# Kernel tuning notes

Measured on AMD Instinct MI355X. Metric: run time of the kernel, lower is better.

## Reference

```python
import jax, jax.numpy as jnp
import numpy as np

EPS = float(np.finfo(np.float32).eps)


def setup_inputs() -> dict:
    key = jax.random.key(0)
    k1, k2, k3, k4 = jax.random.split(key, 4)
    B, M, N = 16, 200000, 200000
    xyzs1 = jax.random.normal(k1, (B, M, 3), dtype=jnp.float32)
    xyzs2 = jax.random.normal(k2, (B, M, 3), dtype=jnp.float32)
    pred_pairs = jax.random.randint(k3, (B, N, 2), 0, M)
    weights = jax.random.uniform(k4, (B, 1, N), dtype=jnp.float32)
    return {"xyzs1": xyzs1, "xyzs2": xyzs2, "pred_pairs": pred_pairs, "weights": weights}


def _weighted_procrustes(X, Y, w):
    # X, Y: [B, N, 3]; w: [B, N, 1]. DGR-style weighted Kabsch/Procrustes.
    W1 = jnp.abs(w).sum(axis=1, keepdims=True)            # [B, 1, 1]
    w_norm = w / (W1 + EPS)                               # [B, N, 1]
    mux = (w_norm * X).sum(axis=1, keepdims=True)         # [B, 1, 3]
    muy = (w_norm * Y).sum(axis=1, keepdims=True)         # [B, 1, 3]
    # Sxy = (Y - muy)^T @ (w_norm * (X - mux)) per sample -> [B, 3, 3]
    Sxy = jnp.einsum('bni,bnj->bij', Y - muy, w_norm * (X - mux))
    U, _, Vh = jnp.linalg.svd(Sxy)                        # Sxy = U diag(s) Vh
    # reflection fix: diag(1, 1, sign(det(U) * det(V)))
    d = jnp.where(jnp.linalg.det(U) * jnp.linalg.det(Vh) < 0, -1.0, 1.0)  # [B]
    S = jnp.concatenate([jnp.ones((X.shape[0], 2), dtype=U.dtype), d[:, None]], axis=1)
    R = (U * S[:, None, :]) @ Vh                          # U @ diag(S) @ V^T
    t = muy[:, 0, :] - jnp.einsum('bij,bj->bi', R, mux[:, 0, :])  # [B, 3]
    return R, t


def reference(xyzs1, xyzs2, pred_pairs, weights):
    w = jnp.transpose(weights, (0, 2, 1))                 # [B, N, 1]
    # batched gather of correspondences
    X = jax.vmap(lambda pts, idx: pts[idx])(xyzs1, pred_pairs[:, :, 0])
    Y = jax.vmap(lambda pts, idx: pts[idx])(xyzs2, pred_pairs[:, :, 1])
    Rs, ts = _weighted_procrustes(X, Y, w)
    ws = w.sum(axis=(1, 2))                               # per-sample weight sums
    return Rs, ts, ws
```

## Files before the change

### kernel.cpp

```cpp
#include <hip/hip_runtime.h>
#include <math.h>

#define BPB 128
#define NACC 17

struct __attribute__((packed, aligned(4))) f4 { float x, y, z, w; };

__global__ __launch_bounds__(256) void wp_partials(
    const float* __restrict__ xyzs1,
    const float* __restrict__ xyzs2,
    const int*   __restrict__ pairs,
    const float* __restrict__ weights,
    float* __restrict__ partials,
    int B, int M, int N)
{
    int b, ib;
    if ((B & 7) == 0) {
        const int grp = blockIdx.x / (8 * BPB);
        const int r   = blockIdx.x % (8 * BPB);
        b  = grp * 8 + (r & 7);
        ib = r >> 3;
    } else {
        b  = blockIdx.x % B;
        ib = blockIdx.x / B;
    }
    const int tid = threadIdx.x;

    const float* __restrict__ x1b = xyzs1 + (size_t)b * M * 3;
    const float* __restrict__ x2b = xyzs2 + (size_t)b * M * 3;
    const unsigned long long* __restrict__ pb =
        (const unsigned long long*)(pairs + (size_t)b * N * 2);
    const float* __restrict__ wb  = weights + (size_t)b * N;

    const bool lastBatch = (b == B - 1);
    const int  M1 = M - 1;

    float acc[NACC];
#pragma unroll
    for (int k = 0; k < NACC; ++k) acc[k] = 0.f;

    for (int n = ib * 256 + tid; n < N; n += BPB * 256) {
        const unsigned long long pw = __builtin_nontemporal_load(pb + n);
        const int ix = (int)(unsigned)(pw & 0xffffffffu);
        const int iy = (int)(unsigned)(pw >> 32);
        const float w = __builtin_nontemporal_load(wb + n);

        float X0, X1, X2, Y0, Y1, Y2;
        {
            const size_t o = 3 * (size_t)ix;
            if (__builtin_expect(lastBatch && ix == M1, 0)) {
                X0 = x1b[o]; X1 = x1b[o + 1]; X2 = x1b[o + 2];
            } else {
                const f4 v = *(const f4*)(x1b + o);
                X0 = v.x; X1 = v.y; X2 = v.z;
            }
        }
        {
            const size_t o = 3 * (size_t)iy;
            if (__builtin_expect(lastBatch && iy == M1, 0)) {
                Y0 = x2b[o]; Y1 = x2b[o + 1]; Y2 = x2b[o + 2];
            } else {
                const f4 v = *(const f4*)(x2b + o);
                Y0 = v.x; Y1 = v.y; Y2 = v.z;
            }
        }

        acc[0] += fabsf(w);
        acc[1] += w;
        acc[2] += w * X0;
        acc[3] += w * X1;
        acc[4] += w * X2;
        const float wy0 = w * Y0, wy1 = w * Y1, wy2 = w * Y2;
        acc[5] += wy0; acc[6] += wy1; acc[7] += wy2;
        acc[8]  += wy0 * X0; acc[9]  += wy0 * X1; acc[10] += wy0 * X2;
        acc[11] += wy1 * X0; acc[12] += wy1 * X1; acc[13] += wy1 * X2;
        acc[14] += wy2 * X0; acc[15] += wy2 * X1; acc[16] += wy2 * X2;
    }

#pragma unroll
    for (int k = 0; k < NACC; ++k) {
#pragma unroll
        for (int off = 32; off > 0; off >>= 1)
            acc[k] += __shfl_down(acc[k], off);
    }

    __shared__ float red[4][NACC];
    const int wave = tid >> 6, lane = tid & 63;
    if (lane == 0) {
#pragma unroll
        for (int k = 0; k < NACC; ++k) red[wave][k] = acc[k];
    }
    __syncthreads();
    if (tid < NACC) {
        const float s = red[0][tid] + red[1][tid] + red[2][tid] + red[3][tid];
        partials[((size_t)b * BPB + ib) * NACC + tid] = s;
    }
}

__global__ __launch_bounds__(64) void wp_finalize(
    const float* __restrict__ partials,
    float* __restrict__ out,
    int B)
{
    const int b = blockIdx.x;
    const int t = threadIdx.x;

    double acc[NACC];
#pragma unroll
    for (int k = 0; k < NACC; ++k) acc[k] = 0.0;

    const float* __restrict__ p = partials + (size_t)b * BPB * NACC;
    for (int i = t; i < BPB; i += 64) {
#pragma unroll
        for (int k = 0; k < NACC; ++k) acc[k] += (double)p[i * NACC + k];
    }
#pragma unroll
    for (int k = 0; k < NACC; ++k) {
#pragma unroll
        for (int off = 32; off > 0; off >>= 1)
            acc[k] += __shfl_down(acc[k], off);
    }

    if (t != 0) return;

    const double EPS = 1.1920928955078125e-07;
    const double W1 = acc[0];
    const double Sw = acc[1];
    const double inv = 1.0 / (W1 + EPS);
    const double mux[3] = {acc[2] * inv, acc[3] * inv, acc[4] * inv};
    const double muy[3] = {acc[5] * inv, acc[6] * inv, acc[7] * inv};
    const double S0 = Sw * inv;
    const double c2 = 2.0 - S0;

    double S[3][3];
#pragma unroll
    for (int i = 0; i < 3; ++i)
#pragma unroll
        for (int j = 0; j < 3; ++j)
            S[i][j] = acc[8 + i * 3 + j] * inv - muy[i] * mux[j] * c2;

    double A[3][3];
#pragma unroll
    for (int i = 0; i < 3; ++i)
#pragma unroll
        for (int j = 0; j < 3; ++j)
            A[i][j] = S[0][i] * S[0][j] + S[1][i] * S[1][j] + S[2][i] * S[2][j];

    double V[3][3] = {{1, 0, 0}, {0, 1, 0}, {0, 0, 1}};
    for (int sweep = 0; sweep < 30; ++sweep) {
        const double offd = fabs(A[0][1]) + fabs(A[0][2]) + fabs(A[1][2]);
        if (offd == 0.0) break;
        for (int pq = 0; pq < 3; ++pq) {
            const int pi = (pq == 2) ? 1 : 0;
            const int qi = (pq == 0) ? 1 : 2;
            const double apq = A[pi][qi];
            if (fabs(apq) < 1e-300) continue;
            const double theta = (A[qi][qi] - A[pi][pi]) / (2.0 * apq);
            const double tt = copysign(1.0, theta) / (fabs(theta) + sqrt(theta * theta + 1.0));
            const double c = 1.0 / sqrt(tt * tt + 1.0);
            const double s = tt * c;
            const int r = 3 - pi - qi;
            const double apq2 = apq;
            A[pi][pi] -= tt * apq2;
            A[qi][qi] += tt * apq2;
            A[pi][qi] = A[qi][pi] = 0.0;
            const double arp = A[r][pi], arq = A[r][qi];
            A[r][pi] = A[pi][r] = c * arp - s * arq;
            A[r][qi] = A[qi][r] = s * arp + c * arq;
#pragma unroll
            for (int k = 0; k < 3; ++k) {
                const double vkp = V[k][pi], vkq = V[k][qi];
                V[k][pi] = c * vkp - s * vkq;
                V[k][qi] = s * vkp + c * vkq;
            }
        }
    }

    double lam[3] = {A[0][0], A[1][1], A[2][2]};
    int idx[3] = {0, 1, 2};
    if (lam[idx[0]] < lam[idx[1]]) { int q = idx[0]; idx[0] = idx[1]; idx[1] = q; }
    if (lam[idx[0]] < lam[idx[2]]) { int q = idx[0]; idx[0] = idx[2]; idx[2] = q; }
    if (lam[idx[1]] < lam[idx[2]]) { int q = idx[1]; idx[1] = idx[2]; idx[2] = q; }

    const double v0[3] = {V[0][idx[0]], V[1][idx[0]], V[2][idx[0]]};
    const double v1[3] = {V[0][idx[1]], V[1][idx[1]], V[2][idx[1]]};

    double u0[3], u1[3];
#pragma unroll
    for (int i = 0; i < 3; ++i) u0[i] = S[i][0] * v0[0] + S[i][1] * v0[1] + S[i][2] * v0[2];
    {
        const double n2 = u0[0] * u0[0] + u0[1] * u0[1] + u0[2] * u0[2];
        const double in0 = 1.0 / sqrt(fmax(n2, 1e-300));
        u0[0] *= in0; u0[1] *= in0; u0[2] *= in0;
    }
#pragma unroll
    for (int i = 0; i < 3; ++i) u1[i] = S[i][0] * v1[0] + S[i][1] * v1[1] + S[i][2] * v1[2];
    {
        const double d01 = u1[0] * u0[0] + u1[1] * u0[1] + u1[2] * u0[2];
        u1[0] -= d01 * u0[0]; u1[1] -= d01 * u0[1]; u1[2] -= d01 * u0[2];
        const double n2 = u1[0] * u1[0] + u1[1] * u1[1] + u1[2] * u1[2];
        const double in1 = 1.0 / sqrt(fmax(n2, 1e-300));
        u1[0] *= in1; u1[1] *= in1; u1[2] *= in1;
    }
    const double u2[3] = {u0[1] * u1[2] - u0[2] * u1[1],
                          u0[2] * u1[0] - u0[0] * u1[2],
                          u0[0] * u1[1] - u0[1] * u1[0]};
    const double v2[3] = {v0[1] * v1[2] - v0[2] * v1[1],
                          v0[2] * v1[0] - v0[0] * v1[2],
                          v0[0] * v1[1] - v0[1] * v1[0]};

    double R[3][3];
#pragma unroll
    for (int i = 0; i < 3; ++i)
#pragma unroll
        for (int j = 0; j < 3; ++j)
            R[i][j] = u0[i] * v0[j] + u1[i] * v1[j] + u2[i] * v2[j];

    double tv[3];
#pragma unroll
    for (int i = 0; i < 3; ++i)
        tv[i] = muy[i] - (R[i][0] * mux[0] + R[i][1] * mux[1] + R[i][2] * mux[2]);

    float* __restrict__ Rout = out + (size_t)b * 9;
#pragma unroll
    for (int i = 0; i < 3; ++i)
#pragma unroll
        for (int j = 0; j < 3; ++j)
            Rout[i * 3 + j] = (float)R[i][j];
    float* __restrict__ tout = out + (size_t)B * 9 + (size_t)b * 3;
#pragma unroll
    for (int i = 0; i < 3; ++i) tout[i] = (float)tv[i];
    out[(size_t)B * 12 + b] = (float)Sw;
}

extern "C" void kernel_launch(void* const* d_in, const int* in_sizes, int n_in,
                              void* d_out, int out_size, void* d_ws, size_t ws_size,
                              hipStream_t stream) {
    const float* xyzs1   = (const float*)d_in[0];
    const float* xyzs2   = (const float*)d_in[1];
    const int*   pairs   = (const int*)d_in[2];
    const float* weights = (const float*)d_in[3];
    float* out = (float*)d_out;

    const int B = out_size / 13;
    const int M = in_sizes[0] / (3 * B);
    const int N = in_sizes[3] / B;

    float* partials = (float*)d_ws;

    hipLaunchKernelGGL(wp_partials, dim3(B * BPB), dim3(256), 0, stream,
                       xyzs1, xyzs2, pairs, weights, partials, B, M, N);
    hipLaunchKernelGGL(wp_finalize, dim3(B), dim3(64), 0, stream,
                       partials, out, B);
}
```

Baseline: 78.97 us.

## Process four correspondences per thread with vectorized index/weight loads

```diff
diff --git a/kernel.cpp b/kernel.cpp
--- a/kernel.cpp
+++ b/kernel.cpp
@@ -1,10 +1,68 @@
 #include <hip/hip_runtime.h>
 #include <math.h>
 
-#define BPB 128
+#define BPB 96
 #define NACC 17
 
+typedef float  floatx4 __attribute__((ext_vector_type(4)));
+typedef unsigned long long ullx2 __attribute__((ext_vector_type(2)));
+
 struct __attribute__((packed, aligned(4))) f4 { float x, y, z, w; };
+
+__device__ __forceinline__ void gather_pt(const float* __restrict__ base, int idx,
+                                          bool guard, int M1,
+                                          float& p0, float& p1, float& p2)
+{
+    const size_t o = 3 * (size_t)idx;
+    if (guard && __builtin_expect(idx == M1, 0)) {
+        p0 = base[o]; p1 = base[o + 1]; p2 = base[o + 2];
+    } else {
+        const f4 v = *(const f4*)(base + o);
+        p0 = v.x; p1 = v.y; p2 = v.z;
+    }
+}
+
+template <bool GUARD>
+__device__ __forceinline__ void wp_loop(
+    const float* __restrict__ x1b, const float* __restrict__ x2b,
+    const ullx2* __restrict__ pv, const floatx4* __restrict__ wv,
+    int c0, int stride, int nChunks, int M1, float acc[NACC])
+{
+    for (int c = c0; c < nChunks; c += stride) {
+        const ullx2  pA = __builtin_nontemporal_load(&pv[2 * c]);
+        const ullx2  pB = __builtin_nontemporal_load(&pv[2 * c + 1]);
+        const floatx4 w4 = __builtin_nontemporal_load(&wv[c]);
+
+        int ix[4], iy[4];
+        ix[0] = (int)(unsigned)(pA.x & 0xffffffffu); iy[0] = (int)(unsigned)(pA.x >> 32);
+        ix[1] = (int)(unsigned)(pA.y & 0xffffffffu); iy[1] = (int)(unsigned)(pA.y >> 32);
+        ix[2] = (int)(unsigned)(pB.x & 0xffffffffu); iy[2] = (int)(unsigned)(pB.x >> 32);
+        ix[3] = (int)(unsigned)(pB.y & 0xffffffffu); iy[3] = (int)(unsigned)(pB.y >> 32);
+
+        float X[4][3], Y[4][3];
+#pragma unroll
+        for (int u = 0; u < 4; ++u)
+            gather_pt(x1b, ix[u], GUARD, M1, X[u][0], X[u][1], X[u][2]);
+#pragma unroll
+        for (int u = 0; u < 4; ++u)
+            gather_pt(x2b, iy[u], GUARD, M1, Y[u][0], Y[u][1], Y[u][2]);
+
+#pragma unroll
+        for (int u = 0; u < 4; ++u) {
+            const float w = w4[u];
+            acc[0] += fabsf(w);
+            acc[1] += w;
+            acc[2] += w * X[u][0];
+            acc[3] += w * X[u][1];
+            acc[4] += w * X[u][2];
+            const float wy0 = w * Y[u][0], wy1 = w * Y[u][1], wy2 = w * Y[u][2];
+            acc[5] += wy0; acc[6] += wy1; acc[7] += wy2;
+            acc[8]  += wy0 * X[u][0]; acc[9]  += wy0 * X[u][1]; acc[10] += wy0 * X[u][2];
+            acc[11] += wy1 * X[u][0]; acc[12] += wy1 * X[u][1]; acc[13] += wy1 * X[u][2];
+            acc[14] += wy2 * X[u][0]; acc[15] += wy2 * X[u][1]; acc[16] += wy2 * X[u][2];
+        }
+    }
+}
 
 __global__ __launch_bounds__(256) void wp_partials(
     const float* __restrict__ xyzs1,
@@ -28,48 +86,33 @@
 
     const float* __restrict__ x1b = xyzs1 + (size_t)b * M * 3;
     const float* __restrict__ x2b = xyzs2 + (size_t)b * M * 3;
-    const unsigned long long* __restrict__ pb =
-        (const unsigned long long*)(pairs + (size_t)b * N * 2);
-    const float* __restrict__ wb  = weights + (size_t)b * N;
+    const ullx2* __restrict__ pv  = (const ullx2*)(pairs + (size_t)b * N * 2);
+    const floatx4* __restrict__ wv = (const floatx4*)(weights + (size_t)b * N);
 
     const bool lastBatch = (b == B - 1);
     const int  M1 = M - 1;
+    const int  nChunks = N >> 2;
 
     float acc[NACC];
 #pragma unroll
     for (int k = 0; k < NACC; ++k) acc[k] = 0.f;
 
-    for (int n = ib * 256 + tid; n < N; n += BPB * 256) {
-        const unsigned long long pw = __builtin_nontemporal_load(pb + n);
-        const int ix = (int)(unsigned)(pw & 0xffffffffu);
-        const int iy = (int)(unsigned)(pw >> 32);
-        const float w = __builtin_nontemporal_load(wb + n);
-
+    const int c0 = ib * 256 + tid;
+    if (lastBatch)
+        wp_loop<true >(x1b, x2b, pv, wv, c0, BPB * 256, nChunks, M1, acc);
+    else
+        wp_loop<false>(x1b, x2b, pv, wv, c0, BPB * 256, nChunks, M1, acc);
+
+    const int* pb = (const int*)pv;
+    const float* wb = (const float*)wv;
+    for (int n = (nChunks << 2) + ib * 256 + tid; n < N; n += BPB * 256) {
+        const int ixt = pb[2 * n], iyt = pb[2 * n + 1];
+        const float w = wb[n];
         float X0, X1, X2, Y0, Y1, Y2;
-        {
-            const size_t o = 3 * (size_t)ix;
-            if (__builtin_expect(lastBatch && ix == M1, 0)) {
-                X0 = x1b[o]; X1 = x1b[o + 1]; X2 = x1b[o + 2];
-            } else {
-                const f4 v = *(const f4*)(x1b + o);
-                X0 = v.x; X1 = v.y; X2 = v.z;
-            }
-        }
-        {
-            const size_t o = 3 * (size_t)iy;
-            if (__builtin_expect(lastBatch && iy == M1, 0)) {
-                Y0 = x2b[o]; Y1 = x2b[o + 1]; Y2 = x2b[o + 2];
-            } else {
-                const f4 v = *(const f4*)(x2b + o);
-                Y0 = v.x; Y1 = v.y; Y2 = v.z;
-            }
-        }
-
-        acc[0] += fabsf(w);
-        acc[1] += w;
-        acc[2] += w * X0;
-        acc[3] += w * X1;
-        acc[4] += w * X2;
+        gather_pt(x1b, ixt, true, M1, X0, X1, X2);
+        gather_pt(x2b, iyt, true, M1, Y0, Y1, Y2);
+        acc[0] += fabsf(w); acc[1] += w;
+        acc[2] += w * X0; acc[3] += w * X1; acc[4] += w * X2;
         const float wy0 = w * Y0, wy1 = w * Y1, wy2 = w * Y2;
         acc[5] += wy0; acc[6] += wy1; acc[7] += wy2;
         acc[8]  += wy0 * X0; acc[9]  += wy0 * X1; acc[10] += wy0 * X2;
@@ -160,9 +203,8 @@
             const double c = 1.0 / sqrt(tt * tt + 1.0);
             const double s = tt * c;
             const int r = 3 - pi - qi;
-            const double apq2 = apq;
-            A[pi][pi] -= tt * apq2;
-            A[qi][qi] += tt * apq2;
+            A[pi][pi] -= tt * apq;
+            A[qi][qi] += tt * apq;
             A[pi][qi] = A[qi][pi] = 0.0;
             const double arp = A[r][pi], arq = A[r][qi];
             A[r][pi] = A[pi][r] = c * arp - s * arq;
```

Result: faster. 72.53 us (-8.2%).
